# Optimization experiments

Measured on AMD Instinct MI355X. Metric: run time of the kernel, lower is better.

## Reference

```python
import jax, jax.numpy as jnp
import numpy as np

B, N, F_IN = 2, 2048, 512
H, DH = 8, 64          # n_heads, n_hidden = out_features // n_heads
SLOPE = 0.2            # LeakyReLU negative slope


def setup_inputs() -> dict:
    key = jax.random.key(0)
    k1, k2, k3 = jax.random.split(key, 3)
    f = jax.random.normal(k1, (B, N, F_IN), dtype=jnp.float32)
    adj_mat = jnp.ones((B, N, N), dtype=bool)  # unused by the original forward
    # linear: Linear(in_features, n_hidden*n_heads, bias=False); store as [in, out]
    W_lin = jax.random.normal(k2, (F_IN, H * DH), dtype=jnp.float32) / np.sqrt(F_IN)
    # attn: Linear(2*n_hidden, 1, bias=False); store as vector [2*n_hidden]
    attn_w = jax.random.normal(k3, (2 * DH,), dtype=jnp.float32) / np.sqrt(2 * DH)
    return {"f": f, "adj_mat": adj_mat, "W_lin": W_lin, "attn_w": attn_w}


def reference(f, adj_mat, W_lin, attn_w):
    b, n, _ = f.shape
    g = (f @ W_lin).reshape(b, n, H, DH)            # [b, n, h, dh]
    # attn(cat[g_i, g_j]) decomposes: e_ij = lrelu(g_i . a_l + g_j . a_r)
    a_l, a_r = attn_w[:DH], attn_w[DH:]
    s_l = jnp.einsum('bihd,d->bih', g, a_l)         # score contribution of node i
    s_r = jnp.einsum('bjhd,d->bjh', g, a_r)         # score contribution of node j
    e = s_l[:, :, None, :] + s_r[:, None, :, :]     # [b, i, j, h]
    e = jnp.where(e >= 0, e, SLOPE * e)             # LeakyReLU(0.2)
    a = jax.nn.softmax(e, axis=2)                   # softmax over dim=-2 (j)
    # dropout is identity in eval mode
    attn_res = jnp.einsum('bijh,bjhf->bihf', a, g)  # [b, i, h, dh]
    return attn_res.reshape(b, n, H * DH)           # is_concat=True
```

## Files before the change

kernel.cpp:

```cpp
#include <hip/hip_runtime.h>
#include <hip/hip_bf16.h>

#define B_ 2
#define N_ 2048
#define FIN 512
#define H_ 8
#define DH 64
#define HD 512
#define SLOPE 0.2f
#define LOG2E 1.44269504088896340736f

typedef __attribute__((ext_vector_type(8))) short short8;
typedef __attribute__((ext_vector_type(4))) float f32x4;
typedef unsigned short ushort_t;

__device__ __forceinline__ ushort_t hi_trunc(float x) {
  return (ushort_t)(__float_as_uint(x) >> 16);
}
__device__ __forceinline__ ushort_t lo_part(float x) {
  const float hf = __uint_as_float(__float_as_uint(x) & 0xFFFF0000u);
  const __hip_bfloat16 lb = __float2bfloat16(x - hf);
  return *(const ushort_t*)&lb;
}
__device__ __forceinline__ ushort_t bf16_rne(float x) {
  const __hip_bfloat16 b = __float2bfloat16(x);
  return *(const ushort_t*)&b;
}

__global__ __launch_bounds__(512) void k_gemm_fused(
    const float* __restrict__ f, const float* __restrict__ W,
    const float* __restrict__ aw, ushort_t* __restrict__ gT,
    float* __restrict__ sl, float* __restrict__ sr,
    float* __restrict__ Bn, float* __restrict__ Dn) {
  __shared__ ushort_t lA[2][2][128 * 64];
  __shared__ ushort_t lB[2][2][64 * 64];
  __shared__ float slp[2][128], srp[2][128];
  const int tid = threadIdx.x;
  const int lane = tid & 63;
  const int wave = tid >> 6;
  const int row0 = blockIdx.x * 128;
  const int col0 = blockIdx.y * 64;
  const int wm = (wave >> 1) * 32;
  const int wn = (wave & 1) * 32;
  const int ar = tid >> 2;
  const int aks = (tid & 3) * 16;
  const int bn = tid & 63;
  const int bks = (tid >> 6) * 8;
  f32x4 acc[2][2] = {};
  float fa[16];
  float fb[8];

#define LOADR(k0)                                                           \
  {                                                                         \
    const float* ap = f + (row0 + ar) * FIN + (k0) + aks;                   \
    _Pragma("unroll") for (int i = 0; i < 4; ++i) {                         \
      const float4 v = *(const float4*)(ap + i * 4);                        \
      fa[i * 4 + 0] = v.x; fa[i * 4 + 1] = v.y;                             \
      fa[i * 4 + 2] = v.z; fa[i * 4 + 3] = v.w;                             \
    }                                                                       \
    _Pragma("unroll") for (int j = 0; j < 8; ++j)                           \
      fb[j] = W[((k0) + bks + j) * HD + col0 + bn];                         \
  }

#define WRITELDS(buf)                                                       \
  {                                                                         \
    _Pragma("unroll") for (int c = 0; c < 2; ++c) {                         \
      short8 hv, lv;                                                        \
      _Pragma("unroll") for (int j = 0; j < 8; ++j) {                       \
        hv[j] = (short)hi_trunc(fa[c * 8 + j]);                             \
        lv[j] = (short)lo_part(fa[c * 8 + j]);                              \
      }                                                                     \
      const int kbA = ((tid & 3) << 5) + (c << 4);                          \
      const int offA = (ar * 128 + (kbA ^ ((ar & 7) << 4))) >> 1;           \
      *(short8*)&lA[buf][0][offA] = hv;                                     \
      *(short8*)&lA[buf][1][offA] = lv;                                     \
    }                                                                       \
    {                                                                       \
      short8 hv, lv;                                                        \
      _Pragma("unroll") for (int j = 0; j < 8; ++j) {                       \
        hv[j] = (short)hi_trunc(fb[j]);                                     \
        lv[j] = (short)lo_part(fb[j]);                                      \
      }                                                                     \
      const int kbB = bks << 1;                                             \
      const int offB = (bn * 128 + (kbB ^ ((bn & 7) << 4))) >> 1;           \
      *(short8*)&lB[buf][0][offB] = hv;                                     \
      *(short8*)&lB[buf][1][offB] = lv;                                     \
    }                                                                       \
  }

  LOADR(0);
  WRITELDS(0);
  __syncthreads();
  int cur = 0;
  for (int t = 0; t < 8; ++t) {
    if (t < 7) LOADR((t + 1) * 64);
#pragma unroll
    for (int kk = 0; kk < 2; ++kk) {
      short8 a_h[2], a_l[2], b_h[2], b_l[2];
      const int kbyte = kk * 64 + ((lane >> 4) << 4);
#pragma unroll
      for (int fm = 0; fm < 2; ++fm) {
        const int row = wm + fm * 16 + (lane & 15);
        const int off = (row * 128 + (kbyte ^ ((row & 7) << 4))) >> 1;
        a_h[fm] = *(const short8*)&lA[cur][0][off];
        a_l[fm] = *(const short8*)&lA[cur][1][off];
      }
#pragma unroll
      for (int fn = 0; fn < 2; ++fn) {
        const int nn = wn + fn * 16 + (lane & 15);
        const int off = (nn * 128 + (kbyte ^ ((nn & 7) << 4))) >> 1;
        b_h[fn] = *(const short8*)&lB[cur][0][off];
        b_l[fn] = *(const short8*)&lB[cur][1][off];
      }
#pragma unroll
      for (int fm = 0; fm < 2; ++fm)
#pragma unroll
        for (int fn = 0; fn < 2; ++fn) {
          acc[fm][fn] = __builtin_amdgcn_mfma_f32_16x16x32_bf16(
              a_h[fm], b_h[fn], acc[fm][fn], 0, 0, 0);
          acc[fm][fn] = __builtin_amdgcn_mfma_f32_16x16x32_bf16(
              a_h[fm], b_l[fn], acc[fm][fn], 0, 0, 0);
          acc[fm][fn] = __builtin_amdgcn_mfma_f32_16x16x32_bf16(
              a_l[fm], b_h[fn], acc[fm][fn], 0, 0, 0);
        }
    }
    if (t < 7) WRITELDS(cur ^ 1);
    __syncthreads();
    cur ^= 1;
  }
#undef LOADR
#undef WRITELDS

  float* T = (float*)lA;
#pragma unroll
  for (int fm = 0; fm < 2; ++fm)
#pragma unroll
    for (int fn = 0; fn < 2; ++fn)
#pragma unroll
      for (int r = 0; r < 4; ++r) {
        const int col = wn + fn * 16 + (lane & 15);
        const int rl = wm + fm * 16 + ((lane >> 4) << 2) + r;
        T[col * 132 + rl] = acc[fm][fn][r];
      }
  __syncthreads();
  {
    const int b = row0 >> 11;
    const int n0 = row0 & (N_ - 1);
    const int d = tid >> 3;
    const int nc = (tid & 7) * 16;
    const size_t gb = ((size_t)((b * H_ + blockIdx.y) * 64 + d)) * N_ + n0 + nc;
#pragma unroll
    for (int half = 0; half < 2; ++half) {
      short8 hv;
#pragma unroll
      for (int u = 0; u < 8; ++u)
        hv[u] = (short)bf16_rne(T[d * 132 + nc + half * 8 + u]);
      *(short8*)&gT[gb + half * 8] = hv;
    }
  }

  const float al0 = aw[wn + (lane & 15)];
  const float al1 = aw[wn + 16 + (lane & 15)];
  const float ar0 = aw[DH + wn + (lane & 15)];
  const float ar1 = aw[DH + wn + 16 + (lane & 15)];
#pragma unroll
  for (int fm = 0; fm < 2; ++fm)
#pragma unroll
    for (int r = 0; r < 4; ++r) {
      float vsl = acc[fm][0][r] * al0 + acc[fm][1][r] * al1;
      float vsr = acc[fm][0][r] * ar0 + acc[fm][1][r] * ar1;
#pragma unroll
      for (int off = 1; off < 16; off <<= 1) {
        vsl += __shfl_xor(vsl, off, 64);
        vsr += __shfl_xor(vsr, off, 64);
      }
      if ((lane & 15) == 0) {
        const int rr = wm + fm * 16 + ((lane >> 4) << 2) + r;
        slp[wn >> 5][rr] = vsl;
        srp[wn >> 5][rr] = vsr;
      }
    }
  __syncthreads();
  if (tid < 128) {
    const int grow = row0 + tid;
    const int b = grow >> 11, n = grow & (N_ - 1);
    const int h = blockIdx.y;
    const int idx = (b * H_ + h) * N_ + n;
    const float srv = srp[0][tid] + srp[1][tid];
    sl[idx] = slp[0][tid] + slp[1][tid];
    sr[idx] = srv;
    Bn[idx] = exp2f(srv * LOG2E);
    Dn[idx] = exp2f(srv * (SLOPE * LOG2E));
  }
}

__global__ __launch_bounds__(256) void k_attn(const ushort_t* __restrict__ gT,
                                              const float* __restrict__ sl,
                                              const float* __restrict__ sr,
                                              const float* __restrict__ Bn,
                                              const float* __restrict__ Dn,
                                              float* __restrict__ out) {
  __shared__ ushort_t ghi[2][64 * 64];
  __shared__ float wred[4];
  const int tid = threadIdx.x;
  const int lane = tid & 63;
  const int wave = tid >> 6;
  const int bh = blockIdx.x;
  const int b = bh >> 3, h = bh & 7;
  const int i0 = blockIdx.y * 64 + wave * 16;
  const int row_l = lane & 15;
  const int kg = lane >> 4;
  const int sd = tid >> 2;
  const int sjb = (tid & 3) * 16;

  float mx = -1e30f;
  for (int q = tid; q < N_; q += 256) mx = fmaxf(mx, sr[bh * N_ + q]);
#pragma unroll
  for (int off = 32; off > 0; off >>= 1) mx = fmaxf(mx, __shfl_xor(mx, off, 64));
  if (lane == 0) wred[wave] = mx;
  __syncthreads();
  mx = fmaxf(fmaxf(wred[0], wred[1]), fmaxf(wred[2], wred[3]));

  const float sli = sl[bh * N_ + i0 + row_l];
  const float pre = sli + mx;
  const float Mi = fmaxf(pre, SLOPE * pre);
  const float Ai = exp2f(fmaf(sli, LOG2E, -Mi * LOG2E));
  const float Ci = exp2f(fmaf(sli, SLOPE * LOG2E, -Mi * LOG2E));

  int ridx[4][2];
#pragma unroll
  for (int gg = 0; gg < 4; ++gg) {
    const int d = gg * 16 + row_l;
#pragma unroll
    for (int kk = 0; kk < 2; ++kk) {
      const int j0r = kk * 32 + kg * 8;
      ridx[gg][kk] = d * 64 + (j0r ^ ((d & 7) << 3));
    }
  }
  const short8 ones = {0x3F80, 0x3F80, 0x3F80, 0x3F80,
                       0x3F80, 0x3F80, 0x3F80, 0x3F80};

  const ushort_t* gH = gT + ((size_t)bh * 64 + sd) * N_ + sjb;
  const float* Bp0 = Bn + bh * N_ + kg * 8;
  const float* Bp1 = Bn + bh * N_ + 32 + kg * 8;
  const float* Dp0 = Dn + bh * N_ + kg * 8;
  const float* Dp1 = Dn + bh * N_ + 32 + kg * 8;

  f32x4 O[4] = {};
  f32x4 Zacc = {};
  short8 sh0, sh1;

#define ALOAD(jb)                                                           \
  {                                                                         \
    sh0 = *(const short8*)&gH[jb];                                          \
    sh1 = *(const short8*)&gH[(jb) + 8];                                    \
  }
#define AWRITE(buf)                                                         \
  {                                                                         \
    const int base_ = sd * 64;                                              \
    const int sw_ = (sd & 7) << 3;                                          \
    *(short8*)&ghi[buf][base_ + (sjb ^ sw_)] = sh0;                         \
    *(short8*)&ghi[buf][base_ + ((sjb + 8) ^ sw_)] = sh1;                   \
  }

  ALOAD(0);
  AWRITE(0);
  __syncthreads();
  int cur = 0;
  for (int t = 0; t < 32; ++t) {
    const int jb = t * 64;
    if (t < 31) ALOAD(jb + 64);
    short8 a[2];
    {
      const float4 b0 = *(const float4*)&Bp0[jb];
      const float4 b1 = *(const float4*)&Bp0[jb + 4];
      const float4 b2 = *(const float4*)&Bp1[jb];
      const float4 b3 = *(const float4*)&Bp1[jb + 4];
      const float4 d0 = *(const float4*)&Dp0[jb];
      const float4 d1 = *(const float4*)&Dp0[jb + 4];
      const float4 d2 = *(const float4*)&Dp1[jb];
      const float4 d3 = *(const float4*)&Dp1[jb + 4];
      const float bs0[8] = {b0.x, b0.y, b0.z, b0.w, b1.x, b1.y, b1.z, b1.w};
      const float ds0[8] = {d0.x, d0.y, d0.z, d0.w, d1.x, d1.y, d1.z, d1.w};
      const float bs1[8] = {b2.x, b2.y, b2.z, b2.w, b3.x, b3.y, b3.z, b3.w};
      const float ds1[8] = {d2.x, d2.y, d2.z, d2.w, d3.x, d3.y, d3.z, d3.w};
#pragma unroll
      for (int u = 0; u < 8; ++u) {
        a[0][u] = (short)bf16_rne(fmaxf(Ai * bs0[u], Ci * ds0[u]));
        a[1][u] = (short)bf16_rne(fmaxf(Ai * bs1[u], Ci * ds1[u]));
      }
    }
    Zacc = __builtin_amdgcn_mfma_f32_16x16x32_bf16(a[0], ones, Zacc, 0, 0, 0);
    Zacc = __builtin_amdgcn_mfma_f32_16x16x32_bf16(a[1], ones, Zacc, 0, 0, 0);
#pragma unroll
    for (int gg = 0; gg < 4; ++gg)
#pragma unroll
      for (int kk = 0; kk < 2; ++kk) {
        const short8 b_h = *(const short8*)&ghi[cur][ridx[gg][kk]];
        O[gg] = __builtin_amdgcn_mfma_f32_16x16x32_bf16(a[kk], b_h, O[gg], 0, 0, 0);
      }
    if (t < 31) AWRITE(cur ^ 1);
    __syncthreads();
    cur ^= 1;
  }
#undef ALOAD
#undef AWRITE
#pragma unroll
  for (int gg = 0; gg < 4; ++gg)
#pragma unroll
    for (int rr = 0; rr < 4; ++rr) {
      const int row = i0 + kg * 4 + rr;
      const int col = h * DH + gg * 16 + row_l;
      out[(b * N_ + row) * HD + col] = O[gg][rr] / Zacc[rr];
    }
}

extern "C" void kernel_launch(void* const* d_in, const int* in_sizes, int n_in,
                              void* d_out, int out_size, void* d_ws, size_t ws_size,
                              hipStream_t stream) {
  const float* f = (const float*)d_in[0];
  const float* W = (const float*)d_in[2];
  const float* aw = (const float*)d_in[3];
  float* out = (float*)d_out;

  ushort_t* gT = (ushort_t*)d_ws;
  float* sl = (float*)(gT + 16 * 64 * N_);
  float* sr = sl + B_ * N_ * H_;
  float* Bn = sr + B_ * N_ * H_;
  float* Dn = Bn + B_ * N_ * H_;

  hipLaunchKernelGGL(k_gemm_fused, dim3((B_ * N_) / 128, HD / 64), dim3(512), 0, stream,
                     f, W, aw, gT, sl, sr, Bn, Dn);
  hipLaunchKernelGGL(k_attn, dim3(B_ * H_, N_ / 64), dim3(256), 0, stream,
                     gT, sl, sr, Bn, Dn, out);
}
```

Before: 47.87 us.

## Triple-buffer LDS tiles and prefetch B/D scales one tile ahead in attention loop

Replaces the double-buffered LDS tile of transposed g with a three-slot ring and issues global loads two tiles ahead using alternating register sets. It also prefetches the per-column Bn/Dn exponent factors one iteration early into registers, and raises wave priority around the MFMA block with s_setprio. The aim is to hide global load latency behind the matrix-core work. In exchange it uses more registers and LDS, which could lower occupancy.

After: 51.69 us. 1.08x slower.

```diff
diff --git a/kernel.cpp b/kernel.cpp
--- a/kernel.cpp
+++ b/kernel.cpp
@@ -200,7 +200,7 @@
                                               const float* __restrict__ Bn,
                                               const float* __restrict__ Dn,
                                               float* __restrict__ out) {
-  __shared__ ushort_t ghi[2][64 * 64];
+  __shared__ ushort_t gbuf[3 * 64 * 64];
   __shared__ float wred[4];
   const int tid = threadIdx.x;
   const int lane = tid & 63;
@@ -248,63 +248,91 @@
 
   f32x4 O[4] = {};
   f32x4 Zacc = {};
-  short8 sh0, sh1;
-
-#define ALOAD(jb)                                                           \
+  short8 sA0, sA1, sB0, sB1;
+  float4 cb0, cb1, cb2, cb3, cd0, cd1, cd2, cd3;
+  float4 pb0, pb1, pb2, pb3, pd0, pd1, pd2, pd3;
+
+  const int wbase = sd * 64;
+  const int sw = (sd & 7) << 3;
+  const int w0 = wbase + (sjb ^ sw);
+  const int w1 = wbase + ((sjb + 8) ^ sw);
+
+#define ALOADA(jb) { sA0 = *(const short8*)&gH[jb]; sA1 = *(const short8*)&gH[(jb) + 8]; }
+#define ALOADB(jb) { sB0 = *(const short8*)&gH[jb]; sB1 = *(const short8*)&gH[(jb) + 8]; }
+#define AWRITEA(bf) { *(short8*)&gbuf[(bf) * 4096 + w0] = sA0; *(short8*)&gbuf[(bf) * 4096 + w1] = sA1; }
+#define AWRITEB(bf) { *(short8*)&gbuf[(bf) * 4096 + w0] = sB0; *(short8*)&gbuf[(bf) * 4096 + w1] = sB1; }
+#define BDLOAD(jb, B0, B1, B2, B3, D0, D1, D2, D3)                          \
   {                                                                         \
-    sh0 = *(const short8*)&gH[jb];                                          \
-    sh1 = *(const short8*)&gH[(jb) + 8];                                    \
-  }
-#define AWRITE(buf)                                                         \
+    B0 = *(const float4*)&Bp0[jb];                                          \
+    B1 = *(const float4*)&Bp0[(jb) + 4];                                    \
+    B2 = *(const float4*)&Bp1[jb];                                          \
+    B3 = *(const float4*)&Bp1[(jb) + 4];                                    \
+    D0 = *(const float4*)&Dp0[jb];                                          \
+    D1 = *(const float4*)&Dp0[(jb) + 4];                                    \
+    D2 = *(const float4*)&Dp1[jb];                                          \
+    D3 = *(const float4*)&Dp1[(jb) + 4];                                    \
+  }
+#define COMPUTE(curbuf)                                                     \
   {                                                                         \
-    const int base_ = sd * 64;                                              \
-    const int sw_ = (sd & 7) << 3;                                          \
-    *(short8*)&ghi[buf][base_ + (sjb ^ sw_)] = sh0;                         \
-    *(short8*)&ghi[buf][base_ + ((sjb + 8) ^ sw_)] = sh1;                   \
-  }
-
-  ALOAD(0);
-  AWRITE(0);
-  __syncthreads();
-  int cur = 0;
-  for (int t = 0; t < 32; ++t) {
-    const int jb = t * 64;
-    if (t < 31) ALOAD(jb + 64);
-    short8 a[2];
-    {
-      const float4 b0 = *(const float4*)&Bp0[jb];
-      const float4 b1 = *(const float4*)&Bp0[jb + 4];
-      const float4 b2 = *(const float4*)&Bp1[jb];
-      const float4 b3 = *(const float4*)&Bp1[jb + 4];
-      const float4 d0 = *(const float4*)&Dp0[jb];
-      const float4 d1 = *(const float4*)&Dp0[jb + 4];
-      const float4 d2 = *(const float4*)&Dp1[jb];
-      const float4 d3 = *(const float4*)&Dp1[jb + 4];
-      const float bs0[8] = {b0.x, b0.y, b0.z, b0.w, b1.x, b1.y, b1.z, b1.w};
-      const float ds0[8] = {d0.x, d0.y, d0.z, d0.w, d1.x, d1.y, d1.z, d1.w};
-      const float bs1[8] = {b2.x, b2.y, b2.z, b2.w, b3.x, b3.y, b3.z, b3.w};
-      const float ds1[8] = {d2.x, d2.y, d2.z, d2.w, d3.x, d3.y, d3.z, d3.w};
-#pragma unroll
-      for (int u = 0; u < 8; ++u) {
-        a[0][u] = (short)bf16_rne(fmaxf(Ai * bs0[u], Ci * ds0[u]));
-        a[1][u] = (short)bf16_rne(fmaxf(Ai * bs1[u], Ci * ds1[u]));
-      }
-    }
-    Zacc = __builtin_amdgcn_mfma_f32_16x16x32_bf16(a[0], ones, Zacc, 0, 0, 0);
-    Zacc = __builtin_amdgcn_mfma_f32_16x16x32_bf16(a[1], ones, Zacc, 0, 0, 0);
-#pragma unroll
-    for (int gg = 0; gg < 4; ++gg)
-#pragma unroll
-      for (int kk = 0; kk < 2; ++kk) {
-        const short8 b_h = *(const short8*)&ghi[cur][ridx[gg][kk]];
-        O[gg] = __builtin_amdgcn_mfma_f32_16x16x32_bf16(a[kk], b_h, O[gg], 0, 0, 0);
-      }
-    if (t < 31) AWRITE(cur ^ 1);
+    short8 a[2];                                                            \
+    {                                                                       \
+      const float bs0[8] = {cb0.x, cb0.y, cb0.z, cb0.w,                     \
+                            cb1.x, cb1.y, cb1.z, cb1.w};                    \
+      const float ds0[8] = {cd0.x, cd0.y, cd0.z, cd0.w,                     \
+                            cd1.x, cd1.y, cd1.z, cd1.w};                    \
+      const float bs1[8] = {cb2.x, cb2.y, cb2.z, cb2.w,                     \
+                            cb3.x, cb3.y, cb3.z, cb3.w};                    \
+      const float ds1[8] = {cd2.x, cd2.y, cd2.z, cd2.w,                     \
+                            cd3.x, cd3.y, cd3.z, cd3.w};                    \
+      _Pragma("unroll") for (int u = 0; u < 8; ++u) {                       \
+        a[0][u] = (short)bf16_rne(fmaxf(Ai * bs0[u], Ci * ds0[u]));         \
+        a[1][u] = (short)bf16_rne(fmaxf(Ai * bs1[u], Ci * ds1[u]));         \
+      }                                                                     \
+    }                                                                       \
+    const ushort_t* lb_ = &gbuf[(curbuf) * 4096];                           \
+    __builtin_amdgcn_s_setprio(1);                                          \
+    Zacc = __builtin_amdgcn_mfma_f32_16x16x32_bf16(a[0], ones, Zacc, 0, 0, 0); \
+    Zacc = __builtin_amdgcn_mfma_f32_16x16x32_bf16(a[1], ones, Zacc, 0, 0, 0); \
+    _Pragma("unroll") for (int gg = 0; gg < 4; ++gg)                        \
+      _Pragma("unroll") for (int kk = 0; kk < 2; ++kk) {                    \
+        const short8 b_h = *(const short8*)&lb_[ridx[gg][kk]];              \
+        O[gg] = __builtin_amdgcn_mfma_f32_16x16x32_bf16(a[kk], b_h, O[gg], 0, 0, 0); \
+      }                                                                     \
+    __builtin_amdgcn_s_setprio(0);                                          \
+  }
+#define BDROT { cb0 = pb0; cb1 = pb1; cb2 = pb2; cb3 = pb3;                 \
+                cd0 = pd0; cd1 = pd1; cd2 = pd2; cd3 = pd3; }
+
+  ALOADA(0);
+  AWRITEA(0);
+  ALOADA(64);
+  BDLOAD(0, cb0, cb1, cb2, cb3, cd0, cd1, cd2, cd3);
+  __syncthreads();
+  int cur = 0, nxt = 1, nx2 = 2;
+  for (int t = 0; t < 32; t += 2) {
+    if (t + 2 < 32) ALOADB((t + 2) * 64);
+    if (t + 1 < 32) BDLOAD((t + 1) * 64, pb0, pb1, pb2, pb3, pd0, pd1, pd2, pd3);
+    COMPUTE(cur);
+    if (t + 1 < 32) AWRITEA(nxt);
+    if (t + 1 < 32) BDROT;
     __syncthreads();
-    cur ^= 1;
-  }
-#undef ALOAD
-#undef AWRITE
+    int tmp = cur; cur = nxt; nxt = nx2; nx2 = tmp;
+    if (t + 3 < 32) ALOADA((t + 3) * 64);
+    if (t + 2 < 32) BDLOAD((t + 2) * 64, pb0, pb1, pb2, pb3, pd0, pd1, pd2, pd3);
+    COMPUTE(cur);
+    if (t + 2 < 32) AWRITEB(nxt);
+    if (t + 2 < 32) BDROT;
+    __syncthreads();
+    tmp = cur; cur = nxt; nxt = nx2; nx2 = tmp;
+  }
+#undef ALOADA
+#undef ALOADB
+#undef AWRITEA
+#undef AWRITEB
+#undef BDLOAD
+#undef COMPUTE
+#undef BDROT
+
 #pragma unroll
   for (int gg = 0; gg < 4; ++gg)
 #pragma unroll
```

## Load V operands directly from global memory instead of LDS double buffer

Applied to the files above, without the earlier changes.

The attention kernel no longer stages the transposed g tile through a swizzled, double-buffered LDS array with a barrier every iteration. Each wave now loads its MFMA B-operand fragments straight from global memory (L2/L1) each step. This removes LDS traffic and per-iteration __syncthreads, but the four waves in a block now each fetch the same V data redundantly, and there is no explicit prefetch to hide global latency.

Measured after the change: 92.93 us. +94.1%, slower.

```diff
diff --git a/kernel.cpp b/kernel.cpp
--- a/kernel.cpp
+++ b/kernel.cpp
@@ -200,7 +200,6 @@
                                               const float* __restrict__ Bn,
                                               const float* __restrict__ Dn,
                                               float* __restrict__ out) {
-  __shared__ ushort_t ghi[2][64 * 64];
   __shared__ float wred[4];
   const int tid = threadIdx.x;
   const int lane = tid & 63;
@@ -210,8 +209,6 @@
   const int i0 = blockIdx.y * 64 + wave * 16;
   const int row_l = lane & 15;
   const int kg = lane >> 4;
-  const int sd = tid >> 2;
-  const int sjb = (tid & 3) * 16;
 
   float mx = -1e30f;
   for (int q = tid; q < N_; q += 256) mx = fmaxf(mx, sr[bh * N_ + q]);
@@ -227,20 +224,13 @@
   const float Ai = exp2f(fmaf(sli, LOG2E, -Mi * LOG2E));
   const float Ci = exp2f(fmaf(sli, SLOPE * LOG2E, -Mi * LOG2E));
 
-  int ridx[4][2];
-#pragma unroll
-  for (int gg = 0; gg < 4; ++gg) {
-    const int d = gg * 16 + row_l;
-#pragma unroll
-    for (int kk = 0; kk < 2; ++kk) {
-      const int j0r = kk * 32 + kg * 8;
-      ridx[gg][kk] = d * 64 + (j0r ^ ((d & 7) << 3));
-    }
-  }
   const short8 ones = {0x3F80, 0x3F80, 0x3F80, 0x3F80,
                        0x3F80, 0x3F80, 0x3F80, 0x3F80};
 
-  const ushort_t* gH = gT + ((size_t)bh * 64 + sd) * N_ + sjb;
+  const ushort_t* vrow0 = gT + ((size_t)bh * 64 + 0 * 16 + row_l) * N_ + kg * 8;
+  const ushort_t* vrow1 = gT + ((size_t)bh * 64 + 1 * 16 + row_l) * N_ + kg * 8;
+  const ushort_t* vrow2 = gT + ((size_t)bh * 64 + 2 * 16 + row_l) * N_ + kg * 8;
+  const ushort_t* vrow3 = gT + ((size_t)bh * 64 + 3 * 16 + row_l) * N_ + kg * 8;
   const float* Bp0 = Bn + bh * N_ + kg * 8;
   const float* Bp1 = Bn + bh * N_ + 32 + kg * 8;
   const float* Dp0 = Dn + bh * N_ + kg * 8;
@@ -248,28 +238,17 @@
 
   f32x4 O[4] = {};
   f32x4 Zacc = {};
-  short8 sh0, sh1;
-
-#define ALOAD(jb)                                                           \
-  {                                                                         \
-    sh0 = *(const short8*)&gH[jb];                                          \
-    sh1 = *(const short8*)&gH[(jb) + 8];                                    \
-  }
-#define AWRITE(buf)                                                         \
-  {                                                                         \
-    const int base_ = sd * 64;                                              \
-    const int sw_ = (sd & 7) << 3;                                          \
-    *(short8*)&ghi[buf][base_ + (sjb ^ sw_)] = sh0;                         \
-    *(short8*)&ghi[buf][base_ + ((sjb + 8) ^ sw_)] = sh1;                   \
-  }
-
-  ALOAD(0);
-  AWRITE(0);
-  __syncthreads();
-  int cur = 0;
+
   for (int t = 0; t < 32; ++t) {
     const int jb = t * 64;
-    if (t < 31) ALOAD(jb + 64);
+    const short8 v00 = *(const short8*)&vrow0[jb];
+    const short8 v01 = *(const short8*)&vrow0[jb + 32];
+    const short8 v10 = *(const short8*)&vrow1[jb];
+    const short8 v11 = *(const short8*)&vrow1[jb + 32];
+    const short8 v20 = *(const short8*)&vrow2[jb];
+    const short8 v21 = *(const short8*)&vrow2[jb + 32];
+    const short8 v30 = *(const short8*)&vrow3[jb];
+    const short8 v31 = *(const short8*)&vrow3[jb + 32];
     short8 a[2];
     {
       const float4 b0 = *(const float4*)&Bp0[jb];
@@ -292,19 +271,16 @@
     }
     Zacc = __builtin_amdgcn_mfma_f32_16x16x32_bf16(a[0], ones, Zacc, 0, 0, 0);
     Zacc = __builtin_amdgcn_mfma_f32_16x16x32_bf16(a[1], ones, Zacc, 0, 0, 0);
-#pragma unroll
-    for (int gg = 0; gg < 4; ++gg)
-#pragma unroll
-      for (int kk = 0; kk < 2; ++kk) {
-        const short8 b_h = *(const short8*)&ghi[cur][ridx[gg][kk]];
-        O[gg] = __builtin_amdgcn_mfma_f32_16x16x32_bf16(a[kk], b_h, O[gg], 0, 0, 0);
-      }
-    if (t < 31) AWRITE(cur ^ 1);
-    __syncthreads();
-    cur ^= 1;
-  }
-#undef ALOAD
-#undef AWRITE
+    O[0] = __builtin_amdgcn_mfma_f32_16x16x32_bf16(a[0], v00, O[0], 0, 0, 0);
+    O[0] = __builtin_amdgcn_mfma_f32_16x16x32_bf16(a[1], v01, O[0], 0, 0, 0);
+    O[1] = __builtin_amdgcn_mfma_f32_16x16x32_bf16(a[0], v10, O[1], 0, 0, 0);
+    O[1] = __builtin_amdgcn_mfma_f32_16x16x32_bf16(a[1], v11, O[1], 0, 0, 0);
+    O[2] = __builtin_amdgcn_mfma_f32_16x16x32_bf16(a[0], v20, O[2], 0, 0, 0);
+    O[2] = __builtin_amdgcn_mfma_f32_16x16x32_bf16(a[1], v21, O[2], 0, 0, 0);
+    O[3] = __builtin_amdgcn_mfma_f32_16x16x32_bf16(a[0], v30, O[3], 0, 0, 0);
+    O[3] = __builtin_amdgcn_mfma_f32_16x16x32_bf16(a[1], v31, O[3], 0, 0, 0);
+  }
+
 #pragma unroll
   for (int gg = 0; gg < 4; ++gg)
 #pragma unroll
```
